# Performance work log

Measured on AMD Instinct MI355X. Metric: run time of the kernel, lower is better.

The kernel has to match this reference:

```python
import jax, jax.numpy as jnp
import numpy as np

B, S, D, H = 2, 2048, 1024, 16
HD = D // H  # head_dim = 64


def setup_inputs() -> dict:
    key = jax.random.key(0)
    ks = jax.random.split(key, 12)
    s = 1.0 / np.sqrt(D)
    return {
        "query": jax.random.normal(ks[0], (B, S, D), jnp.float32),
        "key": jax.random.normal(ks[1], (B, S, D), jnp.float32),
        "value": jax.random.normal(ks[2], (B, S, D), jnp.float32),
        "attention_mask": jnp.zeros((B, S, S), jnp.float32),
        "WQ_w": jax.random.normal(ks[3], (D, D), jnp.float32) * s,
        "WQ_b": jnp.zeros((D,), jnp.float32),
        "WK_w": jax.random.normal(ks[4], (D, D), jnp.float32) * s,
        "WK_b": jnp.zeros((D,), jnp.float32),
        "WV_w": jax.random.normal(ks[5], (D, D), jnp.float32) * s,
        "WV_b": jnp.zeros((D,), jnp.float32),
        "WO_w": jax.random.normal(ks[6], (D, D), jnp.float32) * s,
        "WO_b": jnp.zeros((D,), jnp.float32),
    }


def _split_heads(x):
    # [B,S,D] -> [B,H,S,HD]
    b, s, _ = x.shape
    return x.reshape(b, s, H, HD).transpose(0, 2, 1, 3)


def reference(query, key, value, attention_mask,
              WQ_w, WQ_b, WK_w, WK_b, WV_w, WV_b, WO_w, WO_b):
    Q = _split_heads(query @ WQ_w.T + WQ_b)   # [B,H,S,HD]
    K = _split_heads(key @ WK_w.T + WK_b)
    V = _split_heads(value @ WV_w.T + WV_b)
    scale = 1.0 / jnp.sqrt(jnp.float32(HD))
    scores = jnp.einsum('bhqd,bhkd->bhqk', Q, K) * scale
    scores = scores + attention_mask[:, None, :, :]
    attn = jax.nn.softmax(scores, axis=-1)    # dropout_prob=0.0 -> identity
    out = jnp.einsum('bhqk,bhkd->bhqd', attn, V)
    out = out.transpose(0, 2, 1, 3).reshape(query.shape[0], -1, D)
    return out @ WO_w.T + WO_b
```

## Files before the change

### kernel.cpp

```cpp
#include <hip/hip_runtime.h>
#include <math.h>


typedef _Float16 h8 __attribute__((ext_vector_type(8)));
typedef _Float16 h4 __attribute__((ext_vector_type(4)));
typedef float f4 __attribute__((ext_vector_type(4)));

#define MFMA16(a, b, c) __builtin_amdgcn_mfma_f32_16x16x32_f16((a), (b), (c), 0, 0, 0)

static constexpr int Bn = 2, Sn = 2048, Dn = 1024, Hn = 16, HDn = 64;
static constexpr int Mn = Bn * Sn;
static constexpr int Kn = Dn;
static constexpr int Nn = Dn;
static constexpr int LDA = 72;
static constexpr int LDC = 136;

__device__ __forceinline__ void gload_lds16(const _Float16* g, _Float16* l) {
  __builtin_amdgcn_global_load_lds(
      (const __attribute__((address_space(1))) unsigned int*)g,
      (__attribute__((address_space(3))) unsigned int*)l, 16, 0, 0);
}

struct CvtJobs {
  const float* src[7];
  _Float16* dst[7];
  int n4[7];
};

__global__ __launch_bounds__(256) void cvt_kernel(CvtJobs j) {
  const int stride = gridDim.x * blockDim.x;
  const int t0 = blockIdx.x * blockDim.x + threadIdx.x;
#pragma unroll
  for (int k = 0; k < 7; ++k) {
    const float4* __restrict__ s = (const float4*)j.src[k];
    h4* __restrict__ d = (h4*)j.dst[k];
    const int n = j.n4[k];
    for (int i = t0; i < n; i += stride) {
      const float4 f = s[i];
      h4 h;
      h[0] = (_Float16)f.x; h[1] = (_Float16)f.y;
      h[2] = (_Float16)f.z; h[3] = (_Float16)f.w;
      d[i] = h;
    }
  }
}

struct QkvArgs {
  const _Float16* X[3];
  const _Float16* W[3];
  const float* bias[3];
  _Float16* out[3];
};

__global__ __launch_bounds__(256) void gemm_qkv(QkvArgs args) {
  const int z = blockIdx.z;
  const _Float16* __restrict__ X = args.X[z];
  const _Float16* __restrict__ W = args.W[z];
  const float* __restrict__ bias = args.bias[z];
  _Float16* __restrict__ out = args.out[z];
  const float oscale = (z == 0) ? 0.125f : 1.0f;

  __shared__ _Float16 smem[128 * LDC];
  _Float16* As = smem;
  _Float16* Bs = smem + 128 * 64;

  const int t = threadIdx.x;
  const int lane = t & 63, wv = t >> 6;
  const int l15 = lane & 15, quad = lane >> 4;
  const int wm = (wv >> 1) * 64, wn = (wv & 1) * 64;
  const int n0 = blockIdx.x * 128, m0 = blockIdx.y * 128;

  f4 acc[4][4];
#pragma unroll
  for (int i = 0; i < 4; ++i)
#pragma unroll
    for (int j = 0; j < 4; ++j) {
      f4 zz = {0.f, 0.f, 0.f, 0.f};
      acc[i][j] = zz;
    }

  const int srow = lane >> 3, scol = (lane & 7) * 8;

  for (int k0 = 0; k0 < Kn; k0 += 64) {
    __syncthreads();
#pragma unroll
    for (int u = 0; u < 4; ++u) {
      const int s = wv * 4 + u;
      const int row = s * 8 + srow;
      gload_lds16(X + (size_t)(m0 + row) * Kn + k0 + scol, As + s * 512);
      gload_lds16(W + (size_t)(n0 + row) * Kn + k0 + scol, Bs + s * 512);
    }
    __syncthreads();
#pragma unroll
    for (int kk = 0; kk < 64; kk += 32) {
      h8 af[4], bfr[4];
#pragma unroll
      for (int i = 0; i < 4; ++i)
        af[i] = *(const h8*)&As[(wm + i * 16 + l15) * 64 + kk + quad * 8];
#pragma unroll
      for (int j = 0; j < 4; ++j)
        bfr[j] = *(const h8*)&Bs[(wn + j * 16 + l15) * 64 + kk + quad * 8];
#pragma unroll
      for (int i = 0; i < 4; ++i)
#pragma unroll
        for (int j = 0; j < 4; ++j)
          acc[i][j] = MFMA16(af[i], bfr[j], acc[i][j]);
    }
  }

  __syncthreads();
  if (z != 2) {
#pragma unroll
    for (int j = 0; j < 4; ++j) {
      const float bv = bias[n0 + wn + j * 16 + l15] * oscale;
#pragma unroll
      for (int i = 0; i < 4; ++i)
#pragma unroll
        for (int r = 0; r < 4; ++r)
          smem[(wm + i * 16 + quad * 4 + r) * LDC + wn + j * 16 + l15] =
              (_Float16)(acc[i][j][r] * oscale + bv);
    }
    __syncthreads();
    const int ml = t >> 1, seg = (t & 1) * 64;
    const int m = m0 + ml;
    const int bb = m >> 11, ss = m & (Sn - 1);
#pragma unroll
    for (int u = 0; u < 8; ++u) {
      const int n = n0 + seg + u * 8;
      const int hh = n >> 6, hd = n & 63;
      *(uint4*)(out + (((size_t)(bb * Hn + hh)) * Sn + ss) * HDn + hd) =
          *(const uint4*)&smem[ml * LDC + seg + u * 8];
    }
  } else {
#pragma unroll
    for (int j = 0; j < 4; ++j) {
      const float bv = bias[n0 + wn + j * 16 + l15];
#pragma unroll
      for (int i = 0; i < 4; ++i) {
        h4 hv;
#pragma unroll
        for (int r = 0; r < 4; ++r) hv[r] = (_Float16)(acc[i][j][r] + bv);
        *(h4*)&smem[(wn + j * 16 + l15) * LDC + wm + i * 16 + quad * 4] = hv;
      }
    }
    __syncthreads();
    const int nl = t >> 1, seg = (t & 1) * 64;
    const int n = n0 + nl;
    const int hh = n >> 6, hd = n & 63;
    const int bb = (m0 + seg) >> 11;
#pragma unroll
    for (int u = 0; u < 8; ++u) {
      const int ss = (m0 + seg + u * 8) & (Sn - 1);
      *(uint4*)(out + (((size_t)(bb * Hn + hh)) * HDn + hd) * Sn + ss) =
          *(const uint4*)&smem[nl * LDC + seg + u * 8];
    }
  }
}

__global__ __launch_bounds__(256) void gemm_o(const _Float16* __restrict__ X,
                                              const _Float16* __restrict__ W,
                                              const float* __restrict__ bias,
                                              float* __restrict__ out) {
  __shared__ _Float16 As[128 * 64];
  __shared__ _Float16 Bs[128 * 64];

  const int t = threadIdx.x;
  const int lane = t & 63, wv = t >> 6;
  const int l15 = lane & 15, quad = lane >> 4;
  const int wm = (wv >> 1) * 64, wn = (wv & 1) * 64;
  const int n0 = blockIdx.x * 128, m0 = blockIdx.y * 128;

  f4 acc[4][4];
#pragma unroll
  for (int i = 0; i < 4; ++i)
#pragma unroll
    for (int j = 0; j < 4; ++j) {
      f4 zz = {0.f, 0.f, 0.f, 0.f};
      acc[i][j] = zz;
    }

  const int srow = lane >> 3, scol = (lane & 7) * 8;

  for (int k0 = 0; k0 < Kn; k0 += 64) {
    __syncthreads();
#pragma unroll
    for (int u = 0; u < 4; ++u) {
      const int s = wv * 4 + u;
      const int row = s * 8 + srow;
      gload_lds16(X + (size_t)(m0 + row) * Kn + k0 + scol, As + s * 512);
      gload_lds16(W + (size_t)(n0 + row) * Kn + k0 + scol, Bs + s * 512);
    }
    __syncthreads();
#pragma unroll
    for (int kk = 0; kk < 64; kk += 32) {
      h8 af[4], bfr[4];
#pragma unroll
      for (int i = 0; i < 4; ++i)
        af[i] = *(const h8*)&As[(wm + i * 16 + l15) * 64 + kk + quad * 8];
#pragma unroll
      for (int j = 0; j < 4; ++j)
        bfr[j] = *(const h8*)&Bs[(wn + j * 16 + l15) * 64 + kk + quad * 8];
#pragma unroll
      for (int i = 0; i < 4; ++i)
#pragma unroll
        for (int j = 0; j < 4; ++j)
          acc[i][j] = MFMA16(af[i], bfr[j], acc[i][j]);
    }
  }

#pragma unroll
  for (int j = 0; j < 4; ++j) {
    const int n = n0 + wn + j * 16 + l15;
    const float bv = bias[n];
#pragma unroll
    for (int i = 0; i < 4; ++i) {
      const int mb = m0 + wm + i * 16 + quad * 4;
#pragma unroll
      for (int r = 0; r < 4; ++r)
        out[(size_t)(mb + r) * Nn + n] = acc[i][j][r] + bv;
    }
  }
}

__global__ __launch_bounds__(256) void attn_kernel(
    const _Float16* __restrict__ Qh,
    const _Float16* __restrict__ Kh,
    const _Float16* __restrict__ Vt,
    const float* __restrict__ mask,
    _Float16* __restrict__ out) {
  __shared__ _Float16 Kl[64 * LDA];
  __shared__ _Float16 Vl[64 * LDA];
  __shared__ _Float16 Pl[4 * 16 * LDA];

  const int t = threadIdx.x;
  const int w = t >> 6, lane = t & 63;
  const int l15 = lane & 15, quad = lane >> 4;

  const int bh = blockIdx.y;
  const int b = bh >> 4, h = bh & 15;
  const size_t headoff = (size_t)bh * Sn * HDn;
  const _Float16* Qp = Qh + headoff;
  const _Float16* Kp = Kh + headoff;
  const _Float16* Vp = Vt + headoff;

  const int qb = blockIdx.x * 64;
  const int q0 = qb + w * 16;
  const h8 qf0 = *(const h8*)(Qp + (size_t)(q0 + l15) * HDn + quad * 8);
  const h8 qf1 = *(const h8*)(Qp + (size_t)(q0 + l15) * HDn + 32 + quad * 8);

  const float* mrow = mask + ((size_t)b * Sn + q0 + l15) * Sn;

  float m_run = -INFINITY, l_run = 0.f;
  f4 o_acc[4];
#pragma unroll
  for (int nt = 0; nt < 4; ++nt) {
    f4 zz = {0.f, 0.f, 0.f, 0.f};
    o_acc[nt] = zz;
  }

  _Float16* Pw = &Pl[(w * 16) * LDA];

  for (int kt = 0; kt < Sn / 64; ++kt) {
    __syncthreads();
#pragma unroll
    for (int u = 0; u < 2; ++u) {
      const int c = t + u * 256;
      const int row = c >> 3, c8 = (c & 7) * 8;
      *(uint4*)&Kl[row * LDA + c8] =
          *(const uint4*)(Kp + (size_t)(kt * 64 + row) * HDn + c8);
      *(uint4*)&Vl[row * LDA + c8] =
          *(const uint4*)(Vp + (size_t)row * Sn + kt * 64 + c8);
    }
    __syncthreads();

    f4 s[4];
#pragma unroll
    for (int ks = 0; ks < 4; ++ks) {
      const h8 kf0 = *(const h8*)&Kl[(ks * 16 + l15) * LDA + quad * 8];
      const h8 kf1 = *(const h8*)&Kl[(ks * 16 + l15) * LDA + 32 + quad * 8];
      f4 a = {0.f, 0.f, 0.f, 0.f};
      a = MFMA16(kf0, qf0, a);
      a = MFMA16(kf1, qf1, a);
      const float4 mv = *(const float4*)(mrow + kt * 64 + ks * 16 + quad * 4);
#pragma unroll
      for (int r = 0; r < 4; ++r) s[ks][r] = a[r] + ((const float*)&mv)[r];
    }

    float mx = s[0][0];
#pragma unroll
    for (int ks = 0; ks < 4; ++ks)
#pragma unroll
      for (int r = 0; r < 4; ++r) mx = fmaxf(mx, s[ks][r]);
    mx = fmaxf(mx, __shfl_xor(mx, 16));
    mx = fmaxf(mx, __shfl_xor(mx, 32));
    const float nm = fmaxf(m_run, mx);
    const float alpha = __expf(m_run - nm);
    m_run = nm;
    float sm = 0.f;
#pragma unroll
    for (int ks = 0; ks < 4; ++ks)
#pragma unroll
      for (int r = 0; r < 4; ++r) {
        s[ks][r] = __expf(s[ks][r] - nm);
        sm += s[ks][r];
      }
    sm += __shfl_xor(sm, 16);
    sm += __shfl_xor(sm, 32);
    l_run = l_run * alpha + sm;
#pragma unroll
    for (int nt = 0; nt < 4; ++nt)
#pragma unroll
      for (int r = 0; r < 4; ++r) o_acc[nt][r] *= alpha;

#pragma unroll
    for (int ks = 0; ks < 4; ++ks) {
      h4 pv;
#pragma unroll
      for (int r = 0; r < 4; ++r) pv[r] = (_Float16)s[ks][r];
      *(h4*)&Pw[l15 * LDA + ks * 16 + quad * 4] = pv;
    }

#pragma unroll
    for (int kk = 0; kk < 64; kk += 32) {
      const h8 pf = *(const h8*)&Pw[l15 * LDA + kk + quad * 8];
#pragma unroll
      for (int nt = 0; nt < 4; ++nt) {
        const h8 vf = *(const h8*)&Vl[(nt * 16 + l15) * LDA + kk + quad * 8];
        o_acc[nt] = MFMA16(vf, pf, o_acc[nt]);
      }
    }
  }

  const float rl = 1.0f / l_run;
#pragma unroll
  for (int nt = 0; nt < 4; ++nt) {
    h4 ov;
#pragma unroll
    for (int r = 0; r < 4; ++r) ov[r] = (_Float16)(o_acc[nt][r] * rl);
    *(h4*)&Pw[l15 * LDA + nt * 16 + quad * 4] = ov;
  }
  const int qr = lane >> 2;
  const int seg = (lane & 3) * 16;
  const int qg = q0 + qr;
  _Float16* dst = out + ((size_t)b * Sn + qg) * Dn + h * 64 + seg;
  *(uint4*)dst = *(const uint4*)&Pw[qr * LDA + seg];
  *(uint4*)(dst + 8) = *(const uint4*)&Pw[qr * LDA + seg + 8];
}

extern "C" void kernel_launch(void* const* d_in, const int* in_sizes, int n_in,
                              void* d_out, int out_size, void* d_ws, size_t ws_size,
                              hipStream_t stream) {
  const float* q = (const float*)d_in[0];
  const float* k = (const float*)d_in[1];
  const float* v = (const float*)d_in[2];
  const float* mask = (const float*)d_in[3];
  const float* WQ = (const float*)d_in[4];
  const float* bQ = (const float*)d_in[5];
  const float* WK = (const float*)d_in[6];
  const float* bK = (const float*)d_in[7];
  const float* WV = (const float*)d_in[8];
  const float* bV = (const float*)d_in[9];
  const float* WO = (const float*)d_in[10];
  const float* bO = (const float*)d_in[11];

  _Float16* ws = (_Float16*)d_ws;
  const size_t MD = (size_t)Mn * Dn;
  const size_t DD = (size_t)Dn * Dn;
  _Float16* qh  = ws;
  _Float16* kh  = ws + MD;
  _Float16* vh  = ws + 2 * MD;
  _Float16* WQh = ws + 3 * MD;
  _Float16* WKh = WQh + DD;
  _Float16* WVh = WKh + DD;
  _Float16* WOh = WVh + DD;
  _Float16* Qh  = ws + 3 * MD + 4 * DD;
  _Float16* Kh  = Qh + MD;
  _Float16* Vt  = Kh + MD;
  _Float16* AO  = qh;

  CvtJobs cj;
  cj.src[0] = q;  cj.dst[0] = qh;  cj.n4[0] = (int)(MD / 4);
  cj.src[1] = k;  cj.dst[1] = kh;  cj.n4[1] = (int)(MD / 4);
  cj.src[2] = v;  cj.dst[2] = vh;  cj.n4[2] = (int)(MD / 4);
  cj.src[3] = WQ; cj.dst[3] = WQh; cj.n4[3] = (int)(DD / 4);
  cj.src[4] = WK; cj.dst[4] = WKh; cj.n4[4] = (int)(DD / 4);
  cj.src[5] = WV; cj.dst[5] = WVh; cj.n4[5] = (int)(DD / 4);
  cj.src[6] = WO; cj.dst[6] = WOh; cj.n4[6] = (int)(DD / 4);
  cvt_kernel<<<1024, 256, 0, stream>>>(cj);

  QkvArgs ga;
  ga.X[0] = qh; ga.W[0] = WQh; ga.bias[0] = bQ; ga.out[0] = Qh;
  ga.X[1] = kh; ga.W[1] = WKh; ga.bias[1] = bK; ga.out[1] = Kh;
  ga.X[2] = vh; ga.W[2] = WVh; ga.bias[2] = bV; ga.out[2] = Vt;
  gemm_qkv<<<dim3(Nn / 128, Mn / 128, 3), 256, 0, stream>>>(ga);

  attn_kernel<<<dim3(Sn / 64, Bn * Hn), 256, 0, stream>>>(Qh, Kh, Vt, mask, AO);

  gemm_o<<<dim3(Nn / 128, Mn / 128), 256, 0, stream>>>(AO, WOh, bO, (float*)d_out);
}
```

Before: 300.3 us.

## Double-buffer attention K/V via async LDS loads, use exp2 softmax, direct QKV stores

The attention loop now double-buffers K and V tiles in LDS using global_load_lds async copies, issuing the next tile's load before computing on the current one, so memory latency overlaps compute and one barrier per iteration is removed. Softmax switches to exp2 by folding log2(e) into the Q scaling and the mask fma. The QKV GEMM epilogue drops its LDS staging pass and writes directly to global memory, which saves barriers and LDS but gives narrower, less coalesced stores. The unpadded K/V LDS tiles (stride 64) may cause bank conflicts on fragment reads.

```diff
diff --git a/kernel.cpp b/kernel.cpp
--- a/kernel.cpp
+++ b/kernel.cpp
@@ -7,13 +7,14 @@
 typedef float f4 __attribute__((ext_vector_type(4)));
 
 #define MFMA16(a, b, c) __builtin_amdgcn_mfma_f32_16x16x32_f16((a), (b), (c), 0, 0, 0)
+#define EXP2F(x) __builtin_amdgcn_exp2f(x)
 
 static constexpr int Bn = 2, Sn = 2048, Dn = 1024, Hn = 16, HDn = 64;
 static constexpr int Mn = Bn * Sn;
 static constexpr int Kn = Dn;
 static constexpr int Nn = Dn;
-static constexpr int LDA = 72;
-static constexpr int LDC = 136;
+static constexpr int LDP = 72;
+static constexpr float LOG2E = 1.4426950408889634f;
 
 __device__ __forceinline__ void gload_lds16(const _Float16* g, _Float16* l) {
   __builtin_amdgcn_global_load_lds(
@@ -58,11 +59,9 @@
   const _Float16* __restrict__ W = args.W[z];
   const float* __restrict__ bias = args.bias[z];
   _Float16* __restrict__ out = args.out[z];
-  const float oscale = (z == 0) ? 0.125f : 1.0f;
-
-  __shared__ _Float16 smem[128 * LDC];
-  _Float16* As = smem;
-  _Float16* Bs = smem + 128 * 64;
+
+  __shared__ _Float16 As[128 * 64];
+  __shared__ _Float16 Bs[128 * 64];
 
   const int t = threadIdx.x;
   const int lane = t & 63, wv = t >> 6;
@@ -108,51 +107,40 @@
     }
   }
 
-  __syncthreads();
+  const float osc = (z == 0) ? (0.125f * LOG2E) : 1.0f;
   if (z != 2) {
 #pragma unroll
     for (int j = 0; j < 4; ++j) {
-      const float bv = bias[n0 + wn + j * 16 + l15] * oscale;
-#pragma unroll
-      for (int i = 0; i < 4; ++i)
-#pragma unroll
-        for (int r = 0; r < 4; ++r)
-          smem[(wm + i * 16 + quad * 4 + r) * LDC + wn + j * 16 + l15] =
-              (_Float16)(acc[i][j][r] * oscale + bv);
-    }
-    __syncthreads();
-    const int ml = t >> 1, seg = (t & 1) * 64;
-    const int m = m0 + ml;
-    const int bb = m >> 11, ss = m & (Sn - 1);
-#pragma unroll
-    for (int u = 0; u < 8; ++u) {
-      const int n = n0 + seg + u * 8;
+      const int n = n0 + wn + j * 16 + l15;
+      const float bvs = bias[n] * osc;
       const int hh = n >> 6, hd = n & 63;
-      *(uint4*)(out + (((size_t)(bb * Hn + hh)) * Sn + ss) * HDn + hd) =
-          *(const uint4*)&smem[ml * LDC + seg + u * 8];
+#pragma unroll
+      for (int i = 0; i < 4; ++i) {
+        const int mb = m0 + wm + i * 16 + quad * 4;
+        const int bb = mb >> 11;
+#pragma unroll
+        for (int r = 0; r < 4; ++r) {
+          const int ss = (mb + r) & (Sn - 1);
+          out[(((size_t)(bb * Hn + hh)) * Sn + ss) * HDn + hd] =
+              (_Float16)(acc[i][j][r] * osc + bvs);
+        }
+      }
     }
   } else {
 #pragma unroll
     for (int j = 0; j < 4; ++j) {
-      const float bv = bias[n0 + wn + j * 16 + l15];
+      const int n = n0 + wn + j * 16 + l15;
+      const float bv = bias[n];
+      const int hh = n >> 6, hd = n & 63;
 #pragma unroll
       for (int i = 0; i < 4; ++i) {
+        const int mb = m0 + wm + i * 16 + quad * 4;
+        const int bb = mb >> 11, ss = mb & (Sn - 1);
         h4 hv;
 #pragma unroll
         for (int r = 0; r < 4; ++r) hv[r] = (_Float16)(acc[i][j][r] + bv);
-        *(h4*)&smem[(wn + j * 16 + l15) * LDC + wm + i * 16 + quad * 4] = hv;
+        *(h4*)(out + (((size_t)(bb * Hn + hh)) * HDn + hd) * Sn + ss) = hv;
       }
-    }
-    __syncthreads();
-    const int nl = t >> 1, seg = (t & 1) * 64;
-    const int n = n0 + nl;
-    const int hh = n >> 6, hd = n & 63;
-    const int bb = (m0 + seg) >> 11;
-#pragma unroll
-    for (int u = 0; u < 8; ++u) {
-      const int ss = (m0 + seg + u * 8) & (Sn - 1);
-      *(uint4*)(out + (((size_t)(bb * Hn + hh)) * HDn + hd) * Sn + ss) =
-          *(const uint4*)&smem[nl * LDC + seg + u * 8];
     }
   }
 }
@@ -228,9 +216,9 @@
     const _Float16* __restrict__ Vt,
     const float* __restrict__ mask,
     _Float16* __restrict__ out) {
-  __shared__ _Float16 Kl[64 * LDA];
-  __shared__ _Float16 Vl[64 * LDA];
-  __shared__ _Float16 Pl[4 * 16 * LDA];
+  __shared__ _Float16 Kl[2][64 * 64];
+  __shared__ _Float16 Vl[2][64 * 64];
+  __shared__ _Float16 Pl[4 * 16 * LDP];
 
   const int t = threadIdx.x;
   const int w = t >> 6, lane = t & 63;
@@ -258,32 +246,41 @@
     o_acc[nt] = zz;
   }
 
-  _Float16* Pw = &Pl[(w * 16) * LDA];
+  _Float16* Pw = &Pl[(w * 16) * LDP];
+
+  const int r8 = lane >> 3, c8 = (lane & 7) * 8;
+  auto stage = [&](int kt, int bufi) {
+#pragma unroll
+    for (int u = 0; u < 2; ++u) {
+      const int s = w * 2 + u;
+      gload_lds16(Kp + (size_t)(kt * 64 + s * 8 + r8) * HDn + c8,
+                  &Kl[bufi][s * 512]);
+      gload_lds16(Vp + (size_t)(s * 8 + r8) * Sn + kt * 64 + c8,
+                  &Vl[bufi][s * 512]);
+    }
+  };
+
+  stage(0, 0);
 
   for (int kt = 0; kt < Sn / 64; ++kt) {
-    __syncthreads();
-#pragma unroll
-    for (int u = 0; u < 2; ++u) {
-      const int c = t + u * 256;
-      const int row = c >> 3, c8 = (c & 7) * 8;
-      *(uint4*)&Kl[row * LDA + c8] =
-          *(const uint4*)(Kp + (size_t)(kt * 64 + row) * HDn + c8);
-      *(uint4*)&Vl[row * LDA + c8] =
-          *(const uint4*)(Vp + (size_t)row * Sn + kt * 64 + c8);
-    }
-    __syncthreads();
+    const int cur = kt & 1;
+    __syncthreads();
+    if (kt + 1 < Sn / 64) stage(kt + 1, cur ^ 1);
+    const _Float16* Kc = Kl[cur];
+    const _Float16* Vc = Vl[cur];
 
     f4 s[4];
 #pragma unroll
     for (int ks = 0; ks < 4; ++ks) {
-      const h8 kf0 = *(const h8*)&Kl[(ks * 16 + l15) * LDA + quad * 8];
-      const h8 kf1 = *(const h8*)&Kl[(ks * 16 + l15) * LDA + 32 + quad * 8];
+      const h8 kf0 = *(const h8*)&Kc[(ks * 16 + l15) * 64 + quad * 8];
+      const h8 kf1 = *(const h8*)&Kc[(ks * 16 + l15) * 64 + 32 + quad * 8];
       f4 a = {0.f, 0.f, 0.f, 0.f};
       a = MFMA16(kf0, qf0, a);
       a = MFMA16(kf1, qf1, a);
       const float4 mv = *(const float4*)(mrow + kt * 64 + ks * 16 + quad * 4);
 #pragma unroll
-      for (int r = 0; r < 4; ++r) s[ks][r] = a[r] + ((const float*)&mv)[r];
+      for (int r = 0; r < 4; ++r)
+        s[ks][r] = fmaf(((const float*)&mv)[r], LOG2E, a[r]);
     }
 
     float mx = s[0][0];
@@ -294,14 +291,14 @@
     mx = fmaxf(mx, __shfl_xor(mx, 16));
     mx = fmaxf(mx, __shfl_xor(mx, 32));
     const float nm = fmaxf(m_run, mx);
-    const float alpha = __expf(m_run - nm);
+    const float alpha = EXP2F(m_run - nm);
     m_run = nm;
     float sm = 0.f;
 #pragma unroll
     for (int ks = 0; ks < 4; ++ks)
 #pragma unroll
       for (int r = 0; r < 4; ++r) {
-        s[ks][r] = __expf(s[ks][r] - nm);
+        s[ks][r] = EXP2F(s[ks][r] - nm);
         sm += s[ks][r];
       }
     sm += __shfl_xor(sm, 16);
@@ -317,15 +314,15 @@
       h4 pv;
 #pragma unroll
       for (int r = 0; r < 4; ++r) pv[r] = (_Float16)s[ks][r];
-      *(h4*)&Pw[l15 * LDA + ks * 16 + quad * 4] = pv;
+      *(h4*)&Pw[l15 * LDP + ks * 16 + quad * 4] = pv;
     }
 
 #pragma unroll
     for (int kk = 0; kk < 64; kk += 32) {
-      const h8 pf = *(const h8*)&Pw[l15 * LDA + kk + quad * 8];
+      const h8 pf = *(const h8*)&Pw[l15 * LDP + kk + quad * 8];
 #pragma unroll
       for (int nt = 0; nt < 4; ++nt) {
-        const h8 vf = *(const h8*)&Vl[(nt * 16 + l15) * LDA + kk + quad * 8];
+        const h8 vf = *(const h8*)&Vc[(nt * 16 + l15) * 64 + kk + quad * 8];
         o_acc[nt] = MFMA16(vf, pf, o_acc[nt]);
       }
     }
@@ -337,14 +334,14 @@
     h4 ov;
 #pragma unroll
     for (int r = 0; r < 4; ++r) ov[r] = (_Float16)(o_acc[nt][r] * rl);
-    *(h4*)&Pw[l15 * LDA + nt * 16 + quad * 4] = ov;
+    *(h4*)&Pw[l15 * LDP + nt * 16 + quad * 4] = ov;
   }
   const int qr = lane >> 2;
   const int seg = (lane & 3) * 16;
   const int qg = q0 + qr;
   _Float16* dst = out + ((size_t)b * Sn + qg) * Dn + h * 64 + seg;
-  *(uint4*)dst = *(const uint4*)&Pw[qr * LDA + seg];
-  *(uint4*)(dst + 8) = *(const uint4*)&Pw[qr * LDA + seg + 8];
+  *(uint4*)dst = *(const uint4*)&Pw[qr * LDP + seg];
+  *(uint4*)(dst + 8) = *(const uint4*)&Pw[qr * LDP + seg + 8];
 }
 
 extern "C" void kernel_launch(void* const* d_in, const int* in_sizes, int n_in,
```

Result: slower. 370.4 us (+23.3%).
